# Optimization experiments

Measured on AMD Instinct MI355X. Metric: run time of the kernel, lower is better.

## Reference

```python
import jax, jax.numpy as jnp
import numpy as np

N_POS = 8
EVENT_HORIZON = 0.1
# first N_POS entries of POS_MASS_WEIGHTS: SUBJ,OBJ,VERB,ADJ,ADV,PREP,CONJ,DET
POS_W = jnp.array([0.95, 0.9, 0.85, 0.5, 0.4, 0.2, 0.15, 0.05], dtype=jnp.float32)


def setup_inputs() -> dict:
    L, d = 4096, 2048
    key = jax.random.key(0)
    ks = jax.random.split(key, 8)
    s = 1.0 / np.sqrt(d)
    return {
        "token_vecs": jax.random.normal(ks[0], (L, d), dtype=jnp.float32),
        "pos_idx": jax.random.randint(ks[1], (L,), 0, N_POS, dtype=jnp.int64) if jax.config.jax_enable_x64 else jax.random.randint(ks[1], (L,), 0, N_POS),
        "depth": jax.random.randint(ks[2], (L,), 0, 6, dtype=jnp.int32),
        "slot_idx": jax.random.randint(ks[3], (L,), 0, 16, dtype=jnp.int32),
        "token_pos": jnp.arange(L, dtype=jnp.float32),
        "confidences": jax.random.uniform(ks[4], (L,), dtype=jnp.float32),
        "resonances": jax.random.uniform(ks[5], (L,), dtype=jnp.float32),
        "G_micro": jnp.full((N_POS, N_POS), 0.1, dtype=jnp.float32),
        "G_macro": jnp.asarray(0.5, dtype=jnp.float32),
        "k_spring": jnp.full((N_POS,), 0.05, dtype=jnp.float32),
        "temperature": jnp.asarray(1.0, dtype=jnp.float32),
        "Wv_w": jax.random.normal(ks[6], (d, d), dtype=jnp.float32) * s,
        "Wv_b": jnp.zeros((d,), dtype=jnp.float32),
        "Wout_w": jax.random.normal(ks[7], (d, d), dtype=jnp.float32) * s,
        "Wout_b": jnp.zeros((d,), dtype=jnp.float32),
    }


def reference(token_vecs, pos_idx, depth, slot_idx, token_pos, confidences,
              resonances, G_micro, G_macro, k_spring, temperature,
              Wv_w, Wv_b, Wout_w, Wout_b):
    L = token_vecs.shape[0]
    pidx = pos_idx % N_POS
    depth_f = depth.astype(jnp.float32)
    slot_f = slot_idx.astype(jnp.float32)

    # semantic masses: ||v|| * POS weight * (1 + resonance)
    w = POS_W[pidx]
    norms = jnp.linalg.norm(token_vecs, axis=-1)  # (L,)
    masses = norms * w * (1.0 + resonances)

    # black-hole force
    gap = jnp.maximum(confidences - EVENT_HORIZON, 1e-6)
    bh = -0.01 / gap ** 2
    collapsed = confidences <= EVENT_HORIZON
    bh = jnp.where(collapsed, -1e6, bh)

    mm = masses[:, None] * masses[None, :]  # (L,L) m_i * m_j

    # micro gravity: sigmoid(G_micro)[pi,pj] * mi*mj / slot_dist^2
    G_k = jax.nn.sigmoid(G_micro)[pidx[:, None], pidx[None, :]]
    sd = jnp.maximum(jnp.abs(slot_f[:, None] - slot_f[None, :]), 1.0)
    f_micro = G_k * mm / sd ** 2

    # macro gravity: sigmoid(G_macro) * mi*mj / (|di-dj|+1)^2
    dd = jnp.abs(depth_f[:, None] - depth_f[None, :]) + 1.0
    f_macro = jax.nn.sigmoid(G_macro) * mm / dd ** 2

    # spring force: sigmoid(k_spring[pos_i]) * token_dist
    k_pi = jax.nn.sigmoid(k_spring)[pidx]
    td = jnp.abs(token_pos[:, None] - token_pos[None, :])
    f_spring = k_pi[:, None] * td

    scores = f_micro + f_macro + f_spring + bh[:, None] + bh[None, :]
    scores = jnp.where(collapsed[:, None], -1e6, scores)  # collapsed query rows
    eye = jnp.eye(L, dtype=bool)
    scores = jnp.where(eye, 0.0, scores)

    T = jnp.maximum(jnp.abs(temperature), 0.1)
    A = jax.nn.softmax(scores / T, axis=-1)

    V = token_vecs @ Wv_w.T + Wv_b
    out = (A @ V) @ Wout_w.T + Wout_b
    return out, A, scores
```

## Files before the change

### kernel.cpp

```cpp
#include <hip/hip_runtime.h>
#include <math.h>


typedef __attribute__((ext_vector_type(8))) short bf16x8;
typedef __attribute__((ext_vector_type(4))) float f32x4;

__constant__ float POS_W[8] = {0.95f, 0.9f, 0.85f, 0.5f, 0.4f, 0.2f, 0.15f, 0.05f};

__device__ __forceinline__ float sigmoidf(float x) { return 1.0f / (1.0f + expf(-x)); }

__device__ __forceinline__ unsigned short f2bf(float x) {
  unsigned int u = __float_as_uint(x);
  unsigned int r = (u + 0x7fffu + ((u >> 16) & 1u)) >> 16;
  return (unsigned short)r;
}
__device__ __forceinline__ float bf2f(unsigned short h) {
  return __uint_as_float(((unsigned int)h) << 16);
}

__device__ __forceinline__ void load_lds16(const unsigned short* g, unsigned short* l) {
  __builtin_amdgcn_global_load_lds(
      (const __attribute__((address_space(1))) void*)g,
      (__attribute__((address_space(3))) void*)l, 16, 0, 0);
}

__global__ __launch_bounds__(256) void fusedX_kernel(
    const float* __restrict__ tv, const int* __restrict__ pos_idx,
    const float* __restrict__ conf, const float* __restrict__ reso,
    const float* __restrict__ k_spring,
    unsigned short* __restrict__ Xh, unsigned short* __restrict__ Xl,
    float* __restrict__ masses, float* __restrict__ bh, float* __restrict__ kpis,
    int L, int d) {
  int i = blockIdx.x;
  int tid = threadIdx.x;
  const float* row = tv + (size_t)i * d;
  unsigned short* hrow = Xh + (size_t)i * d;
  unsigned short* lrow = Xl + (size_t)i * d;
  float s = 0.0f;
  for (int c = tid * 4; c < d; c += 1024) {
    float4 v = *(const float4*)(row + c);
    s = fmaf(v.x, v.x, fmaf(v.y, v.y, fmaf(v.z, v.z, fmaf(v.w, v.w, s))));
    ushort4 h, l;
    h.x = f2bf(v.x); l.x = f2bf(v.x - bf2f(h.x));
    h.y = f2bf(v.y); l.y = f2bf(v.y - bf2f(h.y));
    h.z = f2bf(v.z); l.z = f2bf(v.z - bf2f(h.z));
    h.w = f2bf(v.w); l.w = f2bf(v.w - bf2f(h.w));
    *(ushort4*)(hrow + c) = h;
    *(ushort4*)(lrow + c) = l;
  }
  for (int o = 32; o > 0; o >>= 1) s += __shfl_down(s, o);
  __shared__ float red[4];
  int wid = tid >> 6, lane = tid & 63;
  if (lane == 0) red[wid] = s;
  __syncthreads();
  if (tid == 0) {
    float total = red[0] + red[1] + red[2] + red[3];
    float norm = sqrtf(total);
    int p = pos_idx[i] & 7;
    masses[i] = norm * POS_W[p] * (1.0f + reso[i]);
    float c0 = conf[i];
    float gap = fmaxf(c0 - 0.1f, 1e-6f);
    float b = -0.01f / (gap * gap);
    if (c0 <= 0.1f) b = -1e6f;
    bh[i] = b;
    kpis[i] = sigmoidf(k_spring[p]);
  }
}

__global__ __launch_bounds__(256) void decompose_kernel(
    const float* __restrict__ src, unsigned short* __restrict__ hi,
    unsigned short* __restrict__ lo, int n) {
  int i = (blockIdx.x * 256 + threadIdx.x) * 4;
  if (i >= n) return;
  float4 v = *(const float4*)&src[i];
  ushort4 h, l;
  h.x = f2bf(v.x); l.x = f2bf(v.x - bf2f(h.x));
  h.y = f2bf(v.y); l.y = f2bf(v.y - bf2f(h.y));
  h.z = f2bf(v.z); l.z = f2bf(v.z - bf2f(h.z));
  h.w = f2bf(v.w); l.w = f2bf(v.w - bf2f(h.w));
  *(ushort4*)&hi[i] = h;
  *(ushort4*)&lo[i] = l;
}

__global__ __launch_bounds__(256) void scores_softmax_kernel(
    const float* __restrict__ masses, const float* __restrict__ bh,
    const float* __restrict__ kpis,
    const int* __restrict__ pos_idx, const int* __restrict__ slot_idx,
    const int* __restrict__ depth, const float* __restrict__ token_pos,
    const float* __restrict__ conf, const float* __restrict__ G_micro,
    const float* __restrict__ G_macro, const float* __restrict__ temperature,
    float* __restrict__ scores, float* __restrict__ A,
    unsigned short* __restrict__ Ahd, unsigned short* __restrict__ Ald, int L) {
  int i = blockIdx.x;
  int tid = threadIdx.x;
  __shared__ float sig_g[64];
  __shared__ float red[4];
  extern __shared__ float srow[];

  if (tid < 64) sig_g[tid] = sigmoidf(G_micro[tid]);

  float sigmac = sigmoidf(G_macro[0]);
  float T = fmaxf(fabsf(temperature[0]), 0.1f);
  float invT = 1.0f / T;

  float m_i = masses[i];
  float bh_i = bh[i];
  float kpi = kpis[i];
  int pi = pos_idx[i] & 7;
  float slot_i = (float)slot_idx[i];
  float depth_i = (float)depth[i];
  float pos_i = token_pos[i];
  bool collapsed_i = conf[i] <= 0.1f;
  __syncthreads();

  float lmax = -INFINITY;
  for (int j = tid; j < L; j += 256) {
    float sc;
    if (j == i) {
      sc = 0.0f;
    } else if (collapsed_i) {
      sc = -1e6f;
    } else {
      int pj = pos_idx[j] & 7;
      float mm = m_i * masses[j];
      float Gk = sig_g[pi * 8 + pj];
      float sd = fmaxf(fabsf(slot_i - (float)slot_idx[j]), 1.0f);
      float f_micro = (Gk * mm) / (sd * sd);
      float dd = fabsf(depth_i - (float)depth[j]) + 1.0f;
      float f_macro = (sigmac * mm) / (dd * dd);
      float f_spring = kpi * fabsf(pos_i - token_pos[j]);
      sc = f_micro + f_macro + f_spring + bh_i + bh[j];
    }
    srow[j] = sc;
    __builtin_nontemporal_store(sc, &scores[(size_t)i * L + j]);
    lmax = fmaxf(lmax, sc);
  }
  for (int o = 32; o > 0; o >>= 1) lmax = fmaxf(lmax, __shfl_down(lmax, o));
  int wid = tid >> 6, lane = tid & 63;
  if (lane == 0) red[wid] = lmax;
  __syncthreads();
  float rowmax = fmaxf(fmaxf(red[0], red[1]), fmaxf(red[2], red[3]));
  __syncthreads();

  float lsum = 0.0f;
  for (int j = tid; j < L; j += 256) {
    float e = expf((srow[j] - rowmax) * invT);
    srow[j] = e;
    lsum += e;
  }
  for (int o = 32; o > 0; o >>= 1) lsum += __shfl_down(lsum, o);
  if (lane == 0) red[wid] = lsum;
  __syncthreads();
  float total = red[0] + red[1] + red[2] + red[3];
  float inv = 1.0f / total;

  for (int j = tid; j < L; j += 256) {
    float a = srow[j] * inv;
    size_t o = (size_t)i * L + j;
    __builtin_nontemporal_store(a, &A[o]);
    unsigned short h = f2bf(a);
    Ahd[o] = h;
    Ald[o] = f2bf(a - bf2f(h));
  }
}

#define GBM 128
#define GBN 128
#define GBK 32

template <int MODE>
__global__ __launch_bounds__(256, 2) void gemm_split_kernel(
    const unsigned short* __restrict__ Ah, const unsigned short* __restrict__ Al,
    const unsigned short* __restrict__ Bh, const unsigned short* __restrict__ Bl,
    const float* __restrict__ bias, float* __restrict__ C,
    unsigned short* __restrict__ Oh, unsigned short* __restrict__ Ol,
    int M, int N, int K) {
  __shared__ unsigned short smem[4][GBM * GBK];
  int tid = threadIdx.x;
  int wave = tid >> 6, lane = tid & 63;
  int wm = wave >> 1, wn = wave & 1;
  int m0 = blockIdx.y * GBM, n0 = blockIdx.x * GBN;

  int lrow = lane >> 2;
  int q = lane & 3;
  int cs = (q ^ ((lrow >> 1) & 3)) * 8;
  const unsigned short* gsrc;
  unsigned short* ldst;
  if (wave == 0)      { gsrc = Ah + (size_t)m0 * K; ldst = &smem[0][0]; }
  else if (wave == 1) { gsrc = Al + (size_t)m0 * K; ldst = &smem[1][0]; }
  else if (wave == 2) { gsrc = Bh + (size_t)n0 * K; ldst = &smem[2][0]; }
  else                { gsrc = Bl + (size_t)n0 * K; ldst = &smem[3][0]; }
  const unsigned short* lane_g = gsrc + (size_t)lrow * K + cs;

  int fr = lane & 15, fg = lane >> 4;
  int rd_col = (fg ^ ((fr >> 1) & 3)) * 8;

  f32x4 zero = {0.0f, 0.0f, 0.0f, 0.0f};
  f32x4 acc[4][4];
#pragma unroll
  for (int a = 0; a < 4; ++a)
#pragma unroll
    for (int b = 0; b < 4; ++b) acc[a][b] = zero;

  for (int k0 = 0; k0 < K; k0 += GBK) {
#pragma unroll
    for (int c = 0; c < 8; ++c) {
      load_lds16(lane_g + (size_t)c * 16 * K + k0, ldst + c * 512);
    }
    __syncthreads();

    bf16x8 a_h[4], a_l[4], b_h[4], b_l[4];
#pragma unroll
    for (int mt = 0; mt < 4; ++mt) {
      int row = wm * 64 + mt * 16 + fr;
      a_h[mt] = *(const bf16x8*)&smem[0][row * GBK + rd_col];
      a_l[mt] = *(const bf16x8*)&smem[1][row * GBK + rd_col];
    }
#pragma unroll
    for (int nt = 0; nt < 4; ++nt) {
      int row = wn * 64 + nt * 16 + fr;
      b_h[nt] = *(const bf16x8*)&smem[2][row * GBK + rd_col];
      b_l[nt] = *(const bf16x8*)&smem[3][row * GBK + rd_col];
    }
#pragma unroll
    for (int mt = 0; mt < 4; ++mt)
#pragma unroll
      for (int nt = 0; nt < 4; ++nt) {
        acc[mt][nt] = __builtin_amdgcn_mfma_f32_16x16x32_bf16(
            a_h[mt], b_h[nt], acc[mt][nt], 0, 0, 0);
        acc[mt][nt] = __builtin_amdgcn_mfma_f32_16x16x32_bf16(
            a_h[mt], b_l[nt], acc[mt][nt], 0, 0, 0);
        acc[mt][nt] = __builtin_amdgcn_mfma_f32_16x16x32_bf16(
            a_l[mt], b_h[nt], acc[mt][nt], 0, 0, 0);
      }
    __syncthreads();
  }

#pragma unroll
  for (int mt = 0; mt < 4; ++mt) {
#pragma unroll
    for (int nt = 0; nt < 4; ++nt) {
      int row0 = m0 + wm * 64 + mt * 16 + fg * 4;
      int col = n0 + wn * 64 + nt * 16 + fr;
      f32x4 v = acc[mt][nt];
      if (MODE == 0) {
        float bv = bias[col];
#pragma unroll
        for (int j = 0; j < 4; ++j)
          __builtin_nontemporal_store(v[j] + bv, &C[(size_t)(row0 + j) * N + col]);
      } else {
#pragma unroll
        for (int j = 0; j < 4; ++j) {
          float x = v[j] + (bias ? bias[row0 + j] : 0.0f);
          unsigned short h = f2bf(x);
          size_t o = (size_t)(row0 + j) * N + col;
          Oh[o] = h;
          Ol[o] = f2bf(x - bf2f(h));
        }
      }
    }
  }
}

extern "C" void kernel_launch(void* const* d_in, const int* in_sizes, int n_in,
                              void* d_out, int out_size, void* d_ws, size_t ws_size,
                              hipStream_t stream) {
  const float* token_vecs = (const float*)d_in[0];
  const int* pos_idx = (const int*)d_in[1];
  const int* depth = (const int*)d_in[2];
  const int* slot_idx = (const int*)d_in[3];
  const float* token_pos = (const float*)d_in[4];
  const float* conf = (const float*)d_in[5];
  const float* reso = (const float*)d_in[6];
  const float* G_micro = (const float*)d_in[7];
  const float* G_macro = (const float*)d_in[8];
  const float* k_spring = (const float*)d_in[9];
  const float* temperature = (const float*)d_in[10];
  const float* Wv_w = (const float*)d_in[11];
  const float* Wv_b = (const float*)d_in[12];
  const float* Wout_w = (const float*)d_in[13];
  const float* Wout_b = (const float*)d_in[14];

  const int L = in_sizes[1];
  const int d = in_sizes[12];

  float* out = (float*)d_out;
  float* A = out + (size_t)L * d;
  float* scores = A + (size_t)L * L;

  float* masses = (float*)d_ws;
  float* bhv = masses + L;
  float* kpis = bhv + L;
  unsigned short* Ahd = (unsigned short*)(kpis + L);
  unsigned short* Ald = Ahd + (size_t)L * L;
  unsigned short* VTh = Ald + (size_t)L * L;
  unsigned short* VTl = VTh + (size_t)d * L;
  unsigned short* Wh = VTl + (size_t)d * L;
  unsigned short* Wl = Wh + (size_t)d * d;
  unsigned short* Xh = Wl + (size_t)d * d;
  unsigned short* Xl = Xh + (size_t)L * d;
  unsigned short* AVh = Xh;
  unsigned short* AVl = Xl;

  fusedX_kernel<<<L, 256, 0, stream>>>(token_vecs, pos_idx, conf, reso, k_spring,
                                       Xh, Xl, masses, bhv, kpis, L, d);

  decompose_kernel<<<(d * d) / 1024, 256, 0, stream>>>(Wv_w, Wh, Wl, d * d);

  scores_softmax_kernel<<<L, 256, L * sizeof(float), stream>>>(
      masses, bhv, kpis, pos_idx, slot_idx, depth, token_pos, conf, G_micro,
      G_macro, temperature, scores, A, Ahd, Ald, L);

  {
    dim3 grid(L / GBN, d / GBM);
    gemm_split_kernel<2><<<grid, 256, 0, stream>>>(Wh, Wl, Xh, Xl, Wv_b,
                                                   nullptr, VTh, VTl, d, L, d);
  }

  decompose_kernel<<<(d * d) / 1024, 256, 0, stream>>>(Wout_w, Wh, Wl, d * d);

  {
    dim3 grid(d / GBN, L / GBM);
    gemm_split_kernel<2><<<grid, 256, 0, stream>>>(Ahd, Ald, VTh, VTl, nullptr,
                                                   nullptr, AVh, AVl, L, d, L);
  }

  {
    dim3 grid(d / GBN, L / GBM);
    gemm_split_kernel<0><<<grid, 256, 0, stream>>>(AVh, AVl, Wh, Wl, Wout_b,
                                                   out, nullptr, nullptr, L, d, d);
  }
}
```

Measured before the change: 672.6 us.

## Pipeline split-bf16 GEMM with double-buffered LDS and serialized hi/lo passes

The split-precision GEMM is restructured. The three hi/lo product passes become one stream of 3*K/64 k-tiles, each loading only one A/B operand pair into a double-buffered LDS stage with BK=64. The next tile is prefetched while the current one runs on MFMA, using explicit vmcnt waits, and MFMA issue priority is raised around the math. The launch also changes to a 1D grid with an XCD-aware chunk remap for better L2 locality. All of this targets load latency and barrier stalls, at the cost of more k-iterations and hand-placed waitcnt logic that relies on the exact count of outstanding loads.

```diff
diff --git a/kernel.cpp b/kernel.cpp
--- a/kernel.cpp
+++ b/kernel.cpp
@@ -164,76 +164,113 @@
   }
 }
 
-#define GBM 128
-#define GBN 128
-#define GBK 32
+#define TBM 128
+#define TBN 128
+#define TBK 64
+#define A_USH (TBM * TBK)
+#define B_USH (TBN * TBK)
+#define BUF_USH (A_USH + B_USH)
 
 template <int MODE>
-__global__ __launch_bounds__(256, 2) void gemm_split_kernel(
+__global__ __launch_bounds__(256, 2) void gemm_pipe_kernel(
     const unsigned short* __restrict__ Ah, const unsigned short* __restrict__ Al,
     const unsigned short* __restrict__ Bh, const unsigned short* __restrict__ Bl,
     const float* __restrict__ bias, float* __restrict__ C,
     unsigned short* __restrict__ Oh, unsigned short* __restrict__ Ol,
-    int M, int N, int K) {
-  __shared__ unsigned short smem[4][GBM * GBK];
-  int tid = threadIdx.x;
-  int wave = tid >> 6, lane = tid & 63;
-  int wm = wave >> 1, wn = wave & 1;
-  int m0 = blockIdx.y * GBM, n0 = blockIdx.x * GBN;
-
-  int lrow = lane >> 2;
-  int q = lane & 3;
-  int cs = (q ^ ((lrow >> 1) & 3)) * 8;
-  const unsigned short* gsrc;
-  unsigned short* ldst;
-  if (wave == 0)      { gsrc = Ah + (size_t)m0 * K; ldst = &smem[0][0]; }
-  else if (wave == 1) { gsrc = Al + (size_t)m0 * K; ldst = &smem[1][0]; }
-  else if (wave == 2) { gsrc = Bh + (size_t)n0 * K; ldst = &smem[2][0]; }
-  else                { gsrc = Bl + (size_t)n0 * K; ldst = &smem[3][0]; }
-  const unsigned short* lane_g = gsrc + (size_t)lrow * K + cs;
-
-  int fr = lane & 15, fg = lane >> 4;
-  int rd_col = (fg ^ ((fr >> 1) & 3)) * 8;
-
-  f32x4 zero = {0.0f, 0.0f, 0.0f, 0.0f};
+    int M, int N, int K, int TM, int TN) {
+  __shared__ unsigned short smem[2][BUF_USH];
+  const int tid = threadIdx.x;
+  const int wave = tid >> 6, lane = tid & 63;
+  const int wm = wave >> 1, wn = wave & 1;
+  const int fr = lane & 15, fg = lane >> 4;
+
+  int bid = blockIdx.x;
+  int chunk = (bid & 7) * (gridDim.x >> 3) + (bid >> 3);
+  int bm = chunk / TN, bn = chunk % TN;
+  int m0 = bm * TBM, n0 = bn * TBN;
+
+  const int lr = lane >> 3;
+  const int lc = lane & 7;
+  const int scol = (lc ^ lr) * 8;
+  size_t laneA[4], laneB[4];
+  int dA[4], dB[4];
+#pragma unroll
+  for (int i = 0; i < 4; ++i) {
+    int arow = wave * 32 + i * 8;
+    laneA[i] = (size_t)(arow + lr) * K + scol;
+    dA[i] = arow * TBK;
+    laneB[i] = (size_t)(arow + lr) * K + scol;
+    dB[i] = A_USH + arow * TBK;
+  }
+
+  int aoff[2][4], boff[2][4];
+#pragma unroll
+  for (int s = 0; s < 2; ++s) {
+#pragma unroll
+    for (int u = 0; u < 4; ++u) {
+      int arow = wm * 64 + u * 16 + fr;
+      aoff[s][u] = arow * TBK + (((s * 4 + fg) ^ (fr & 7)) * 8);
+      int brow = wn * 64 + u * 16 + fr;
+      boff[s][u] = A_USH + brow * TBK + (((s * 4 + fg) ^ (fr & 7)) * 8);
+    }
+  }
+
+  const int tpr = K >> 6;
+  const int NT = 3 * tpr;
+
   f32x4 acc[4][4];
 #pragma unroll
   for (int a = 0; a < 4; ++a)
 #pragma unroll
-    for (int b = 0; b < 4; ++b) acc[a][b] = zero;
-
-  for (int k0 = 0; k0 < K; k0 += GBK) {
-#pragma unroll
-    for (int c = 0; c < 8; ++c) {
-      load_lds16(lane_g + (size_t)c * 16 * K + k0, ldst + c * 512);
-    }
-    __syncthreads();
-
-    bf16x8 a_h[4], a_l[4], b_h[4], b_l[4];
-#pragma unroll
-    for (int mt = 0; mt < 4; ++mt) {
-      int row = wm * 64 + mt * 16 + fr;
-      a_h[mt] = *(const bf16x8*)&smem[0][row * GBK + rd_col];
-      a_l[mt] = *(const bf16x8*)&smem[1][row * GBK + rd_col];
-    }
-#pragma unroll
-    for (int nt = 0; nt < 4; ++nt) {
-      int row = wn * 64 + nt * 16 + fr;
-      b_h[nt] = *(const bf16x8*)&smem[2][row * GBK + rd_col];
-      b_l[nt] = *(const bf16x8*)&smem[3][row * GBK + rd_col];
-    }
-#pragma unroll
-    for (int mt = 0; mt < 4; ++mt)
-#pragma unroll
-      for (int nt = 0; nt < 4; ++nt) {
-        acc[mt][nt] = __builtin_amdgcn_mfma_f32_16x16x32_bf16(
-            a_h[mt], b_h[nt], acc[mt][nt], 0, 0, 0);
-        acc[mt][nt] = __builtin_amdgcn_mfma_f32_16x16x32_bf16(
-            a_h[mt], b_l[nt], acc[mt][nt], 0, 0, 0);
-        acc[mt][nt] = __builtin_amdgcn_mfma_f32_16x16x32_bf16(
-            a_l[mt], b_h[nt], acc[mt][nt], 0, 0, 0);
-      }
-    __syncthreads();
+    for (int b = 0; b < 4; ++b) acc[a][b] = (f32x4){0.f, 0.f, 0.f, 0.f};
+
+  auto stage = [&](int t, int buf) {
+    int r = (t >= 2 * tpr) ? 2 : ((t >= tpr) ? 1 : 0);
+    int koff = (t - r * tpr) << 6;
+    const unsigned short* As = (r < 2) ? Ah : Al;
+    const unsigned short* Bs = (r == 1) ? Bl : Bh;
+    const unsigned short* uA = As + (size_t)m0 * K + koff;
+    const unsigned short* uB = Bs + (size_t)n0 * K + koff;
+    unsigned short* sb = &smem[buf][0];
+#pragma unroll
+    for (int i = 0; i < 4; ++i) load_lds16(uA + laneA[i], sb + dA[i]);
+#pragma unroll
+    for (int i = 0; i < 4; ++i) load_lds16(uB + laneB[i], sb + dB[i]);
+  };
+
+  stage(0, 0);
+
+  for (int t = 0; t < NT; ++t) {
+    const int buf = t & 1;
+    if (t + 1 < NT) {
+      stage(t + 1, buf ^ 1);
+      asm volatile("s_waitcnt vmcnt(8)" ::: "memory");
+    } else {
+      asm volatile("s_waitcnt vmcnt(0)" ::: "memory");
+    }
+    __builtin_amdgcn_s_barrier();
+    asm volatile("" ::: "memory");
+
+    const unsigned short* sb = &smem[buf][0];
+#pragma unroll
+    for (int s = 0; s < 2; ++s) {
+      bf16x8 a[4], b[4];
+#pragma unroll
+      for (int u = 0; u < 4; ++u) a[u] = *(const bf16x8*)&sb[aoff[s][u]];
+#pragma unroll
+      for (int u = 0; u < 4; ++u) b[u] = *(const bf16x8*)&sb[boff[s][u]];
+      __builtin_amdgcn_s_setprio(1);
+#pragma unroll
+      for (int mt = 0; mt < 4; ++mt)
+#pragma unroll
+        for (int nt = 0; nt < 4; ++nt)
+          acc[mt][nt] = __builtin_amdgcn_mfma_f32_16x16x32_bf16(
+              a[mt], b[nt], acc[mt][nt], 0, 0, 0);
+      __builtin_amdgcn_s_setprio(0);
+    }
+    asm volatile("s_waitcnt lgkmcnt(0)" ::: "memory");
+    __builtin_amdgcn_s_barrier();
+    asm volatile("" ::: "memory");
   }
 
 #pragma unroll
@@ -312,22 +349,22 @@
       G_macro, temperature, scores, A, Ahd, Ald, L);
 
   {
-    dim3 grid(L / GBN, d / GBM);
-    gemm_split_kernel<2><<<grid, 256, 0, stream>>>(Wh, Wl, Xh, Xl, Wv_b,
-                                                   nullptr, VTh, VTl, d, L, d);
+    int TM = d / TBM, TN = L / TBN;
+    gemm_pipe_kernel<2><<<TM * TN, 256, 0, stream>>>(
+        Wh, Wl, Xh, Xl, Wv_b, nullptr, VTh, VTl, d, L, d, TM, TN);
   }
 
   decompose_kernel<<<(d * d) / 1024, 256, 0, stream>>>(Wout_w, Wh, Wl, d * d);
 
   {
-    dim3 grid(d / GBN, L / GBM);
-    gemm_split_kernel<2><<<grid, 256, 0, stream>>>(Ahd, Ald, VTh, VTl, nullptr,
-                                                   nullptr, AVh, AVl, L, d, L);
+    int TM = L / TBM, TN = d / TBN;
+    gemm_pipe_kernel<2><<<TM * TN, 256, 0, stream>>>(
+        Ahd, Ald, VTh, VTl, nullptr, nullptr, AVh, AVl, L, d, L, TM, TN);
   }
 
   {
-    dim3 grid(d / GBN, L / GBM);
-    gemm_split_kernel<0><<<grid, 256, 0, stream>>>(AVh, AVl, Wh, Wl, Wout_b,
-                                                   out, nullptr, nullptr, L, d, d);
-  }
-}
+    int TM = L / TBM, TN = d / TBN;
+    gemm_pipe_kernel<0><<<TM * TN, 256, 0, stream>>>(
+        AVh, AVl, Wh, Wl, Wout_b, out, nullptr, nullptr, L, d, d, TM, TN);
+  }
+}
```

New measurement: 657.9 us. 1.02x faster.
